# Performance work log

Measured on AMD Instinct MI355X. Metric: run time of the kernel, lower is better.

## Reference

```python
import jax, jax.numpy as jnp
import numpy as np

B, C, Q, E = 32, 1024, 64, 256  # batch, max_context_len, max_question_len, embedding_size
FE = 4 * E                      # final_encoding_size (self_attention=False)


def setup_inputs() -> dict:
    key = jax.random.key(0)
    ks = jax.random.split(key, 7)
    return {
        "context": jax.random.normal(ks[0], (B, C, E), dtype=jnp.float32),
        "question": jax.random.normal(ks[1], (B, Q, E), dtype=jnp.float32),
        "context_mask": jnp.ones((B, C), dtype=jnp.float32),
        "w_question": jax.random.normal(ks[2], (E,), dtype=jnp.float32),
        "w_context": jax.random.normal(ks[3], (E,), dtype=jnp.float32),
        "w_multiple": jax.random.normal(ks[4], (E,), dtype=jnp.float32),
        "final_W": jax.random.normal(ks[5], (FE, FE), dtype=jnp.float32) * (1.0 / np.sqrt(FE)),
        "final_b": jnp.zeros((FE,), dtype=jnp.float32),
    }


def reference(context, question, context_mask, w_question, w_context, w_multiple, final_W, final_b):
    # Trilinear similarity: s[b,c,q] = <w_q, q_q> + <w_c, c_c> + <w_m, c_c * q_q>
    q_weighted = question @ w_question                 # (B, Q)
    ctx_weighted = context @ w_context                 # (B, C)
    # (question.unsqueeze(1) * context.unsqueeze(2)) @ w_multiple, computed
    # without materializing the (B, C, Q, E) intermediate:
    mult = jnp.einsum('bce,bqe->bcq', context * w_multiple, question)  # (B, C, Q)
    similarity = ctx_weighted[:, :, None] + q_weighted[:, None, :] + mult  # (B, C, Q)

    # Context-to-query attention (softmax over question dim)
    c2q_att = jnp.einsum('bcq,bqe->bce', jax.nn.softmax(similarity, axis=2), question)

    # Query-to-context attention (softmax over context dim of row-max scores)
    q2c_weights = jax.nn.softmax(jnp.max(similarity, axis=2), axis=1)   # (B, C)
    q2c_att = jnp.einsum('bc,bce->be', q2c_weights, context)            # (B, E)

    attended = jnp.concatenate(
        [context, c2q_att, context * c2q_att, context * q2c_att[:, None, :]],
        axis=2)                                                          # (B, C, 4E)

    # MaskedLinear: affine map, output rows zeroed where context_mask == 0
    out = (attended @ final_W.T + final_b) * context_mask[:, :, None]    # (B, C, 4E)
    return out
```

## Files before the change

kernel.cpp:

```cpp
#include <hip/hip_runtime.h>

#define BB 32
#define CC 1024
#define QQ 64
#define EE 256
#define FE 1024
#define MM (BB*CC)

typedef __bf16 bf16_t;
typedef bf16_t bf16x8 __attribute__((ext_vector_type(8)));
typedef float f32x4 __attribute__((ext_vector_type(4)));
typedef unsigned short u16x8 __attribute__((ext_vector_type(8)));

__device__ __forceinline__ unsigned short f2bf(float f) {
  unsigned u = __float_as_uint(f);
  u += 0x7fffu + ((u >> 16) & 1u);
  return (unsigned short)(u >> 16);
}
__device__ __forceinline__ float bf2f(unsigned short u) {
  return __uint_as_float(((unsigned)u) << 16);
}

__device__ __forceinline__ void gload_lds16(const void* g, void* l) {
  __builtin_amdgcn_global_load_lds(
      (const __attribute__((address_space(1))) unsigned int*)g,
      (__attribute__((address_space(3))) unsigned int*)l, 16, 0, 0);
}

__global__ void k_prep(const float* __restrict__ question, const float* __restrict__ w_question,
                       float* __restrict__ qw,
                       const float* __restrict__ W, unsigned short* __restrict__ Wb) {
  int bx = blockIdx.x;
  if (bx < 512) {
    int gid = bx * 256 + threadIdx.x;
    int row = gid >> 6;
    int lane = gid & 63;
    const float4 q = *(const float4*)(question + (size_t)row * EE + lane * 4);
    const float4 wq = *(const float4*)(w_question + lane * 4);
    float d = q.x*wq.x + q.y*wq.y + q.z*wq.z + q.w*wq.w;
    d += __shfl_xor(d, 1);  d += __shfl_xor(d, 2);  d += __shfl_xor(d, 4);
    d += __shfl_xor(d, 8);  d += __shfl_xor(d, 16); d += __shfl_xor(d, 32);
    if (lane == 0) qw[row] = d;
  } else {
    int i = ((bx - 512) * 256 + threadIdx.x) * 4;
    float4 v = *(const float4*)(W + i);
    ushort4 o; o.x = f2bf(v.x); o.y = f2bf(v.y); o.z = f2bf(v.z); o.w = f2bf(v.w);
    *(ushort4*)(Wb + i) = o;
  }
}

#define DOT4(acc, A, Bv) acc += A.x*Bv.x + A.y*Bv.y + A.z*Bv.z + A.w*Bv.w

__launch_bounds__(256)
__global__ void k_simpv(const float* __restrict__ ctx, const float* __restrict__ question,
                        const float* __restrict__ qw_g, const float* __restrict__ w_context,
                        const float* __restrict__ w_multiple,
                        float* __restrict__ rowmax, unsigned short* __restrict__ att) {
  __shared__ float qbuf[QQ * 132];
  __shared__ float ck[64][36];
  __shared__ unsigned short Pl[QQ][68];
  __shared__ float cwl[64];
  __shared__ float qwl[QQ];
  const int tid = threadIdx.x;
  const int b = blockIdx.y;
  const int c0 = blockIdx.x * 64;
  const int tx = tid & 15, ty = tid >> 4;

  const float* qb = question + (size_t)b * (QQ * EE);
  if (tid < QQ) qwl[tid] = qw_g[b * QQ + tid];

  const int cr = tid >> 3, er = (tid & 7) * 4;
  const float* crow0 = ctx + ((size_t)(b * CC + c0 + cr)) * EE;
  const float* crow1 = crow0 + 32 * EE;
  unsigned short* arow0 = att + ((size_t)(b * CC + c0 + cr)) * FE;
  unsigned short* arow1 = arow0 + (size_t)32 * FE;
  float s[4][4] = {{0.f}};
  float cp0 = 0.f, cp1 = 0.f;

  for (int h = 0; h < 2; ++h) {
    if (h) __syncthreads();
    for (int idx = tid * 4; idx < QQ * 128; idx += 1024) {
      int row = idx >> 7, col = idx & 127;
      *(float4*)&qbuf[row * 132 + col] = *(const float4*)(qb + (size_t)row * EE + h * 128 + col);
    }
    for (int eo2 = 0; eo2 < 128; eo2 += 32) {
      const int eo = h * 128 + eo2;
      float4 cv0 = *(const float4*)(crow0 + eo + er);
      float4 cv1 = *(const float4*)(crow1 + eo + er);
      float4 wc = *(const float4*)(w_context + eo + er);
      float4 wm = *(const float4*)(w_multiple + eo + er);
      cp0 += cv0.x*wc.x + cv0.y*wc.y + cv0.z*wc.z + cv0.w*wc.w;
      cp1 += cv1.x*wc.x + cv1.y*wc.y + cv1.z*wc.z + cv1.w*wc.w;
      ushort4 u0, u1;
      u0.x = f2bf(cv0.x); u0.y = f2bf(cv0.y); u0.z = f2bf(cv0.z); u0.w = f2bf(cv0.w);
      u1.x = f2bf(cv1.x); u1.y = f2bf(cv1.y); u1.z = f2bf(cv1.z); u1.w = f2bf(cv1.w);
      *(ushort4*)(arow0 + eo + er) = u0;
      *(ushort4*)(arow1 + eo + er) = u1;
      __syncthreads();
      float4 m0, m1;
      m0.x = cv0.x*wm.x; m0.y = cv0.y*wm.y; m0.z = cv0.z*wm.z; m0.w = cv0.w*wm.w;
      m1.x = cv1.x*wm.x; m1.y = cv1.y*wm.y; m1.z = cv1.z*wm.z; m1.w = cv1.w*wm.w;
      *(float4*)&ck[cr][er] = m0;
      *(float4*)&ck[cr + 32][er] = m1;
      __syncthreads();
#pragma unroll
      for (int ee = 0; ee < 32; ee += 4) {
        float4 a0 = *(const float4*)&ck[ty +  0][ee];
        float4 a1 = *(const float4*)&ck[ty + 16][ee];
        float4 a2 = *(const float4*)&ck[ty + 32][ee];
        float4 a3 = *(const float4*)&ck[ty + 48][ee];
        float4 b0 = *(const float4*)&qbuf[(tx +  0) * 132 + eo2 + ee];
        float4 b1 = *(const float4*)&qbuf[(tx + 16) * 132 + eo2 + ee];
        float4 b2 = *(const float4*)&qbuf[(tx + 32) * 132 + eo2 + ee];
        float4 b3 = *(const float4*)&qbuf[(tx + 48) * 132 + eo2 + ee];
        DOT4(s[0][0], a0, b0); DOT4(s[0][1], a0, b1); DOT4(s[0][2], a0, b2); DOT4(s[0][3], a0, b3);
        DOT4(s[1][0], a1, b0); DOT4(s[1][1], a1, b1); DOT4(s[1][2], a1, b2); DOT4(s[1][3], a1, b3);
        DOT4(s[2][0], a2, b0); DOT4(s[2][1], a2, b1); DOT4(s[2][2], a2, b2); DOT4(s[2][3], a2, b3);
        DOT4(s[3][0], a3, b0); DOT4(s[3][1], a3, b1); DOT4(s[3][2], a3, b2); DOT4(s[3][3], a3, b3);
      }
    }
  }
  cp0 += __shfl_xor(cp0, 1); cp0 += __shfl_xor(cp0, 2); cp0 += __shfl_xor(cp0, 4);
  cp1 += __shfl_xor(cp1, 1); cp1 += __shfl_xor(cp1, 2); cp1 += __shfl_xor(cp1, 4);
  if ((tid & 7) == 0) { cwl[cr] = cp0; cwl[cr + 32] = cp1; }
  __syncthreads();

#pragma unroll
  for (int i = 0; i < 4; ++i) {
    int c = ty + 16 * i;
    float cw = cwl[c];
    float f[4], mx = -1e30f;
#pragma unroll
    for (int j = 0; j < 4; ++j) {
      f[j] = s[i][j] + cw + qwl[tx + 16 * j];
      mx = fmaxf(mx, f[j]);
    }
    mx = fmaxf(mx, __shfl_xor(mx, 1));
    mx = fmaxf(mx, __shfl_xor(mx, 2));
    mx = fmaxf(mx, __shfl_xor(mx, 4));
    mx = fmaxf(mx, __shfl_xor(mx, 8));
    float sum = 0.f;
#pragma unroll
    for (int j = 0; j < 4; ++j) { f[j] = expf(f[j] - mx); sum += f[j]; }
    sum += __shfl_xor(sum, 1);
    sum += __shfl_xor(sum, 2);
    sum += __shfl_xor(sum, 4);
    sum += __shfl_xor(sum, 8);
    float inv = 1.f / sum;
    if (tx == 0) rowmax[(size_t)b * CC + c0 + c] = mx;
#pragma unroll
    for (int j = 0; j < 4; ++j) Pl[tx + 16 * j][c] = f2bf(f[j] * inv);
  }
  __syncthreads();

  for (int ep = 0; ep < EE; ep += 64) {
    if (ep) __syncthreads();
    {
      int q = tid >> 2, e16 = (tid & 3) * 16;
      const float* src = qb + (size_t)q * EE + ep + e16;
      *(float4*)&qbuf[q * 68 + e16 +  0] = *(const float4*)(src);
      *(float4*)&qbuf[q * 68 + e16 +  4] = *(const float4*)(src + 4);
      *(float4*)&qbuf[q * 68 + e16 +  8] = *(const float4*)(src + 8);
      *(float4*)&qbuf[q * 68 + e16 + 12] = *(const float4*)(src + 12);
    }
    __syncthreads();
    float s2[4][4] = {{0.f}};
#pragma unroll 8
    for (int q = 0; q < QQ; ++q) {
      float a0 = bf2f(Pl[q][ty +  0]);
      float a1 = bf2f(Pl[q][ty + 16]);
      float a2 = bf2f(Pl[q][ty + 32]);
      float a3 = bf2f(Pl[q][ty + 48]);
      float4 bv = *(const float4*)&qbuf[q * 68 + tx * 4];
      s2[0][0] += a0 * bv.x; s2[0][1] += a0 * bv.y; s2[0][2] += a0 * bv.z; s2[0][3] += a0 * bv.w;
      s2[1][0] += a1 * bv.x; s2[1][1] += a1 * bv.y; s2[1][2] += a1 * bv.z; s2[1][3] += a1 * bv.w;
      s2[2][0] += a2 * bv.x; s2[2][1] += a2 * bv.y; s2[2][2] += a2 * bv.z; s2[2][3] += a2 * bv.w;
      s2[3][0] += a3 * bv.x; s2[3][1] += a3 * bv.y; s2[3][2] += a3 * bv.z; s2[3][3] += a3 * bv.w;
    }
#pragma unroll
    for (int i = 0; i < 4; ++i) {
      int c = ty + 16 * i;
      size_t row = (size_t)(b * CC + c0 + c);
      unsigned short* arow = att + row * (size_t)FE;
      ushort4 cu = *(const ushort4*)(arow + ep + tx * 4);
      float cx = bf2f(cu.x), cy = bf2f(cu.y), cz = bf2f(cu.z), cw = bf2f(cu.w);
      ushort4 o1, o2;
      o1.x = f2bf(s2[i][0]);       o1.y = f2bf(s2[i][1]);       o1.z = f2bf(s2[i][2]);       o1.w = f2bf(s2[i][3]);
      o2.x = f2bf(cx * s2[i][0]);  o2.y = f2bf(cy * s2[i][1]);  o2.z = f2bf(cz * s2[i][2]);  o2.w = f2bf(cw * s2[i][3]);
      *(ushort4*)(arow + 1 * EE + ep + tx * 4) = o1;
      *(ushort4*)(arow + 2 * EE + ep + tx * 4) = o2;
    }
  }
}

__global__ void k_q2c_softmax(const float* __restrict__ rowmax, float* __restrict__ q2cw) {
  int b = blockIdx.x, tid = threadIdx.x;
  __shared__ float rbuf[4], sbuf[4];
  float4 v = *(const float4*)(rowmax + (size_t)b * CC + tid * 4);
  float m = fmaxf(fmaxf(v.x, v.y), fmaxf(v.z, v.w));
  for (int off = 1; off < 64; off <<= 1) m = fmaxf(m, __shfl_xor(m, off));
  int wv = tid >> 6;
  if ((tid & 63) == 0) rbuf[wv] = m;
  __syncthreads();
  m = fmaxf(fmaxf(rbuf[0], rbuf[1]), fmaxf(rbuf[2], rbuf[3]));
  float e0 = expf(v.x - m), e1 = expf(v.y - m), e2 = expf(v.z - m), e3 = expf(v.w - m);
  float sum = e0 + e1 + e2 + e3;
  for (int off = 1; off < 64; off <<= 1) sum += __shfl_xor(sum, off);
  if ((tid & 63) == 0) sbuf[wv] = sum;
  __syncthreads();
  sum = sbuf[0] + sbuf[1] + sbuf[2] + sbuf[3];
  float inv = 1.f / sum;
  float4 o; o.x = e0 * inv; o.y = e1 * inv; o.z = e2 * inv; o.w = e3 * inv;
  *(float4*)(q2cw + (size_t)b * CC + tid * 4) = o;
}

__global__ void k_q2c_part(const unsigned short* __restrict__ att, const float* __restrict__ w,
                           float* __restrict__ part) {
  int b = blockIdx.y, ch = blockIdx.x;
  int e = threadIdx.x;
  const unsigned short* base = att + ((size_t)(b * CC + ch * 128)) * FE + e;
  const float* wp = w + b * CC + ch * 128;
  float acc = 0.f;
#pragma unroll 4
  for (int c = 0; c < 128; ++c) acc += wp[c] * bf2f(base[(size_t)c * FE]);
  part[(b * 8 + ch) * EE + e] = acc;
}

__global__ void k_q2c_sum(const float* __restrict__ part, float* __restrict__ q2catt) {
  int b = blockIdx.x, e = threadIdx.x;
  float a = 0.f;
#pragma unroll
  for (int ch = 0; ch < 8; ++ch) a += part[(b * 8 + ch) * EE + e];
  q2catt[b * EE + e] = a;
}

__global__ void k_att3(const unsigned short* __restrict__ att_ro, const float* __restrict__ q2catt,
                       unsigned short* __restrict__ att_wr) {
  int unit = blockIdx.x * 256 + threadIdx.x;
  int row = unit >> 5;
  int e8 = (unit & 31) * 8;
  int b = row >> 10;
  u16x8 c = *(const u16x8*)(att_ro + (size_t)row * FE + e8);
  float4 g0 = *(const float4*)(q2catt + b * EE + e8);
  float4 g1 = *(const float4*)(q2catt + b * EE + e8 + 4);
  u16x8 o;
  o[0] = f2bf(bf2f(c[0]) * g0.x); o[1] = f2bf(bf2f(c[1]) * g0.y);
  o[2] = f2bf(bf2f(c[2]) * g0.z); o[3] = f2bf(bf2f(c[3]) * g0.w);
  o[4] = f2bf(bf2f(c[4]) * g1.x); o[5] = f2bf(bf2f(c[5]) * g1.y);
  o[6] = f2bf(bf2f(c[6]) * g1.z); o[7] = f2bf(bf2f(c[7]) * g1.w);
  *(u16x8*)(att_wr + (size_t)row * FE + 3 * EE + e8) = o;
}

__launch_bounds__(512, 2)
__global__ void k_gemm(const unsigned short* __restrict__ A, const unsigned short* __restrict__ Bw,
                       const float* __restrict__ bias, const float* __restrict__ mask,
                       float* __restrict__ out) {
  __shared__ bf16_t As[2][2][128][64];
  __shared__ bf16_t Bs[2][2][128][64];
  const int tid = threadIdx.x;
  const int lane = tid & 63;
  const int wave = tid >> 6;
  const int wr = wave >> 2;
  const int wc = wave & 3;
  const int bh = wc >> 1;

  const int bid = blockIdx.x;
  const int wg = (bid & 7) * 64 + (bid >> 3);
  const int brow = (wg >> 2) * 256;
  const int bcol = (wg & 3) * 256;

  const int r = lane & 15, kg4 = lane >> 4;
  const int rx = r & 7;

  const int srow = tid >> 3;
  const int sg = (tid & 7) ^ (srow & 7);
  const unsigned short* gAb = A  + (size_t)(brow + srow) * FE + sg * 8;
  const unsigned short* gBb = Bw + (size_t)(bcol + srow) * FE + sg * 8;
  bf16_t* ldsAb = &As[0][0][srow][(tid & 7) * 8];
  bf16_t* ldsBb = &Bs[0][0][srow][(tid & 7) * 8];

  f32x4 acc[8][4] = {};
  bf16x8 faA[4][2], faB[4][2], fbA[2][2], fbB[2][2];

#define BARX __builtin_amdgcn_s_barrier()
#define VMW4 asm volatile("s_waitcnt vmcnt(4)" ::: "memory")
#define VMW0 asm volatile("s_waitcnt vmcnt(0)" ::: "memory")

#define ST_A(SLOT, H, KOFF) do {                                              \
    const unsigned short* s_ = gAb + (size_t)((H) * 128) * FE + (KOFF);       \
    bf16_t* d_ = ldsAb + ((SLOT) * 2 + (H)) * (128 * 64);                     \
    gload_lds16(s_, d_);                                                      \
    gload_lds16(s_ + (size_t)64 * FE, d_ + 64 * 64);                          \
  } while (0)
#define ST_B(SLOT, H, KOFF) do {                                              \
    const unsigned short* s_ = gBb + (size_t)((H) * 128) * FE + (KOFF);       \
    bf16_t* d_ = ldsBb + ((SLOT) * 2 + (H)) * (128 * 64);                     \
    gload_lds16(s_, d_);                                                      \
    gload_lds16(s_ + (size_t)64 * FE, d_ + 64 * 64);                          \
  } while (0)

#define RD_FA(DST, SLOT, MB) do {                                             \
    _Pragma("unroll") for (int mm = 0; mm < 4; ++mm) {                        \
      const int row_ = ((MB) + mm) * 16 + r;                                  \
      _Pragma("unroll") for (int ks = 0; ks < 2; ++ks)                        \
        DST[mm][ks] = *(const bf16x8*)&As[SLOT][wr][row_][((ks * 4 + kg4) ^ rx) * 8]; \
    } } while (0)
#define RD_FB(DST, SLOT, NB) do {                                             \
    _Pragma("unroll") for (int nn = 0; nn < 2; ++nn) {                        \
      const int row_ = (wc & 1) * 64 + ((NB) + nn) * 16 + r;                  \
      _Pragma("unroll") for (int ks = 0; ks < 2; ++ks)                        \
        DST[nn][ks] = *(const bf16x8*)&Bs[SLOT][bh][row_][((ks * 4 + kg4) ^ rx) * 8]; \
    } } while (0)

#define MFMA16(FA, FB, MB, NB) do {                                           \
    __builtin_amdgcn_s_setprio(1);                                            \
    _Pragma("unroll") for (int ks = 0; ks < 2; ++ks)                          \
    _Pragma("unroll") for (int mm = 0; mm < 4; ++mm)                          \
    _Pragma("unroll") for (int nn = 0; nn < 2; ++nn)                          \
      acc[(MB) + mm][(NB) + nn] = __builtin_amdgcn_mfma_f32_16x16x32_bf16(    \
          FA[mm][ks], FB[nn][ks], acc[(MB) + mm][(NB) + nn], 0, 0, 0);        \
    __builtin_amdgcn_s_setprio(0);                                            \
  } while (0)

  ST_B(0, 0, 0);  ST_B(0, 1, 0);  ST_A(0, 0, 0);  ST_A(0, 1, 0);
  ST_B(1, 0, 64); ST_B(1, 1, 64);
  VMW4;
  BARX;

#pragma unroll 1
  for (int i = 0; i < 8; ++i) {
    const int kT1 = (2 * i + 1) * 64;
    const int kT2 = (2 * i + 2) * 64;
    const int kT3 = (2 * i + 3) * 64;
    const bool more = (i < 7);

    RD_FA(faA, 0, 0); RD_FB(fbA, 0, 0);
    ST_A(1, 0, kT1);
    BARX; MFMA16(faA, fbA, 0, 0); BARX;
    RD_FB(fbB, 0, 2);
    ST_A(1, 1, kT1);
    BARX; MFMA16(faA, fbB, 0, 2); BARX;
    RD_FA(faB, 0, 4);
    if (more) ST_B(0, 0, kT2);
    BARX; MFMA16(faB, fbA, 4, 0); BARX;
    if (more) { ST_B(0, 1, kT2); VMW4; } else { VMW0; }
    BARX; MFMA16(faB, fbB, 4, 2); BARX;

    RD_FA(faA, 1, 0); RD_FB(fbA, 1, 0);
    if (more) ST_A(0, 0, kT2);
    BARX; MFMA16(faA, fbA, 0, 0); BARX;
    RD_FB(fbB, 1, 2);
    if (more) ST_A(0, 1, kT2);
    BARX; MFMA16(faA, fbB, 0, 2); BARX;
    RD_FA(faB, 1, 4);
    if (more) ST_B(1, 0, kT3);
    BARX; MFMA16(faB, fbA, 4, 0); BARX;
    if (more) { ST_B(1, 1, kT3); VMW4; }
    BARX; MFMA16(faB, fbB, 4, 2); BARX;
  }
#undef ST_A
#undef ST_B
#undef RD_FA
#undef RD_FB
#undef MFMA16

#pragma unroll
  for (int m = 0; m < 8; ++m) {
#pragma unroll
    for (int n = 0; n < 4; ++n) {
#pragma unroll
      for (int reg = 0; reg < 4; ++reg) {
        int row = brow + wr * 128 + m * 16 + kg4 * 4 + reg;
        int col = bcol + wc * 64 + n * 16 + r;
        out[(size_t)row * FE + col] = (acc[m][n][reg] + bias[col]) * mask[row];
      }
    }
  }
}

extern "C" void kernel_launch(void* const* d_in, const int* in_sizes, int n_in,
                              void* d_out, int out_size, void* d_ws, size_t ws_size,
                              hipStream_t stream) {
  const float* ctx  = (const float*)d_in[0];
  const float* ques = (const float*)d_in[1];
  const float* mask = (const float*)d_in[2];
  const float* w_q  = (const float*)d_in[3];
  const float* w_c  = (const float*)d_in[4];
  const float* w_m  = (const float*)d_in[5];
  const float* fW   = (const float*)d_in[6];
  const float* fb   = (const float*)d_in[7];
  float* out = (float*)d_out;

  char* ws = (char*)d_ws;
  float* qw     = (float*)(ws);
  float* rowmax = (float*)(ws + 8192);
  float* q2cw   = (float*)(ws + 139264);
  float* part   = (float*)(ws + 270336);
  float* q2catt = (float*)(ws + 532480);
  unsigned short* attended = (unsigned short*)(ws + 1048576);
  unsigned short* Wb       = (unsigned short*)(ws + 68157440);

  k_prep<<<1536, 256, 0, stream>>>(ques, w_q, qw, fW, Wb);
  k_simpv<<<dim3(16, 32), 256, 0, stream>>>(ctx, ques, qw, w_c, w_m, rowmax, attended);
  k_q2c_softmax<<<32, 256, 0, stream>>>(rowmax, q2cw);
  k_q2c_part<<<dim3(8, 32), 256, 0, stream>>>(attended, q2cw, part);
  k_q2c_sum<<<32, 256, 0, stream>>>(part, q2catt);
  k_att3<<<4096, 256, 0, stream>>>(attended, q2catt, attended);
  k_gemm<<<512, 512, 0, stream>>>(attended, Wb, fb, mask, out);
}
```

Baseline: 160.7 us.

## Replace pipelined 256x256 GEMM with simple single-buffered 128x128 tile kernel

Replaces the hand-scheduled, double-buffered 256x256-tile GEMM (512 threads, K-step 64, interleaved barriers and async LDS loads) with a plain 128x128-tile kernel using 256 threads, K-step 32, a single LDS buffer and two syncthreads per iteration. The grid grows from 512 to 2048 blocks, with more blocks allowed per CU. This trades away load/compute overlap and data reuse per tile for simpler code and more occupancy. It likely exposes global-load latency and doubles operand traffic.

```diff
diff --git a/kernel.cpp b/kernel.cpp
--- a/kernel.cpp
+++ b/kernel.cpp
@@ -251,126 +251,65 @@
   *(u16x8*)(att_wr + (size_t)row * FE + 3 * EE + e8) = o;
 }
 
-__launch_bounds__(512, 2)
+__launch_bounds__(256, 3)
 __global__ void k_gemm(const unsigned short* __restrict__ A, const unsigned short* __restrict__ Bw,
                        const float* __restrict__ bias, const float* __restrict__ mask,
                        float* __restrict__ out) {
-  __shared__ bf16_t As[2][2][128][64];
-  __shared__ bf16_t Bs[2][2][128][64];
+  __shared__ bf16_t As[128][32];
+  __shared__ bf16_t Bs[128][32];
   const int tid = threadIdx.x;
   const int lane = tid & 63;
   const int wave = tid >> 6;
-  const int wr = wave >> 2;
-  const int wc = wave & 3;
-  const int bh = wc >> 1;
+  const int wr = wave >> 1, wc = wave & 1;
 
   const int bid = blockIdx.x;
-  const int wg = (bid & 7) * 64 + (bid >> 3);
-  const int brow = (wg >> 2) * 256;
-  const int bcol = (wg & 3) * 256;
-
-  const int r = lane & 15, kg4 = lane >> 4;
-  const int rx = r & 7;
-
-  const int srow = tid >> 3;
-  const int sg = (tid & 7) ^ (srow & 7);
-  const unsigned short* gAb = A  + (size_t)(brow + srow) * FE + sg * 8;
-  const unsigned short* gBb = Bw + (size_t)(bcol + srow) * FE + sg * 8;
-  bf16_t* ldsAb = &As[0][0][srow][(tid & 7) * 8];
-  bf16_t* ldsBb = &Bs[0][0][srow][(tid & 7) * 8];
-
-  f32x4 acc[8][4] = {};
-  bf16x8 faA[4][2], faB[4][2], fbA[2][2], fbB[2][2];
-
-#define BARX __builtin_amdgcn_s_barrier()
-#define VMW4 asm volatile("s_waitcnt vmcnt(4)" ::: "memory")
-#define VMW0 asm volatile("s_waitcnt vmcnt(0)" ::: "memory")
-
-#define ST_A(SLOT, H, KOFF) do {                                              \
-    const unsigned short* s_ = gAb + (size_t)((H) * 128) * FE + (KOFF);       \
-    bf16_t* d_ = ldsAb + ((SLOT) * 2 + (H)) * (128 * 64);                     \
-    gload_lds16(s_, d_);                                                      \
-    gload_lds16(s_ + (size_t)64 * FE, d_ + 64 * 64);                          \
-  } while (0)
-#define ST_B(SLOT, H, KOFF) do {                                              \
-    const unsigned short* s_ = gBb + (size_t)((H) * 128) * FE + (KOFF);       \
-    bf16_t* d_ = ldsBb + ((SLOT) * 2 + (H)) * (128 * 64);                     \
-    gload_lds16(s_, d_);                                                      \
-    gload_lds16(s_ + (size_t)64 * FE, d_ + 64 * 64);                          \
-  } while (0)
-
-#define RD_FA(DST, SLOT, MB) do {                                             \
-    _Pragma("unroll") for (int mm = 0; mm < 4; ++mm) {                        \
-      const int row_ = ((MB) + mm) * 16 + r;                                  \
-      _Pragma("unroll") for (int ks = 0; ks < 2; ++ks)                        \
-        DST[mm][ks] = *(const bf16x8*)&As[SLOT][wr][row_][((ks * 4 + kg4) ^ rx) * 8]; \
-    } } while (0)
-#define RD_FB(DST, SLOT, NB) do {                                             \
-    _Pragma("unroll") for (int nn = 0; nn < 2; ++nn) {                        \
-      const int row_ = (wc & 1) * 64 + ((NB) + nn) * 16 + r;                  \
-      _Pragma("unroll") for (int ks = 0; ks < 2; ++ks)                        \
-        DST[nn][ks] = *(const bf16x8*)&Bs[SLOT][bh][row_][((ks * 4 + kg4) ^ rx) * 8]; \
-    } } while (0)
-
-#define MFMA16(FA, FB, MB, NB) do {                                           \
-    __builtin_amdgcn_s_setprio(1);                                            \
-    _Pragma("unroll") for (int ks = 0; ks < 2; ++ks)                          \
-    _Pragma("unroll") for (int mm = 0; mm < 4; ++mm)                          \
-    _Pragma("unroll") for (int nn = 0; nn < 2; ++nn)                          \
-      acc[(MB) + mm][(NB) + nn] = __builtin_amdgcn_mfma_f32_16x16x32_bf16(    \
-          FA[mm][ks], FB[nn][ks], acc[(MB) + mm][(NB) + nn], 0, 0, 0);        \
-    __builtin_amdgcn_s_setprio(0);                                            \
-  } while (0)
-
-  ST_B(0, 0, 0);  ST_B(0, 1, 0);  ST_A(0, 0, 0);  ST_A(0, 1, 0);
-  ST_B(1, 0, 64); ST_B(1, 1, 64);
-  VMW4;
-  BARX;
-
-#pragma unroll 1
-  for (int i = 0; i < 8; ++i) {
-    const int kT1 = (2 * i + 1) * 64;
-    const int kT2 = (2 * i + 2) * 64;
-    const int kT3 = (2 * i + 3) * 64;
-    const bool more = (i < 7);
-
-    RD_FA(faA, 0, 0); RD_FB(fbA, 0, 0);
-    ST_A(1, 0, kT1);
-    BARX; MFMA16(faA, fbA, 0, 0); BARX;
-    RD_FB(fbB, 0, 2);
-    ST_A(1, 1, kT1);
-    BARX; MFMA16(faA, fbB, 0, 2); BARX;
-    RD_FA(faB, 0, 4);
-    if (more) ST_B(0, 0, kT2);
-    BARX; MFMA16(faB, fbA, 4, 0); BARX;
-    if (more) { ST_B(0, 1, kT2); VMW4; } else { VMW0; }
-    BARX; MFMA16(faB, fbB, 4, 2); BARX;
-
-    RD_FA(faA, 1, 0); RD_FB(fbA, 1, 0);
-    if (more) ST_A(0, 0, kT2);
-    BARX; MFMA16(faA, fbA, 0, 0); BARX;
-    RD_FB(fbB, 1, 2);
-    if (more) ST_A(0, 1, kT2);
-    BARX; MFMA16(faA, fbB, 0, 2); BARX;
-    RD_FA(faB, 1, 4);
-    if (more) ST_B(1, 0, kT3);
-    BARX; MFMA16(faB, fbA, 4, 0); BARX;
-    if (more) { ST_B(1, 1, kT3); VMW4; }
-    BARX; MFMA16(faB, fbB, 4, 2); BARX;
-  }
-#undef ST_A
-#undef ST_B
-#undef RD_FA
-#undef RD_FB
-#undef MFMA16
-
-#pragma unroll
-  for (int m = 0; m < 8; ++m) {
+  const int wg = (bid & 7) * 256 + (bid >> 3);
+  const int bcol = (wg & 7) * 128;
+  const int brow = (wg >> 3) * 128;
+
+  const int r = lane & 15, kg = lane >> 4;
+  const int rk = (kg ^ (r & 3)) * 8;
+
+  const int srow = tid >> 2;
+  const int sgr = tid & 3;
+  const int ssw = (sgr ^ (srow & 3)) * 8;
+  const unsigned short* gA0 = A  + (size_t)(brow + srow) * FE + ssw;
+  const unsigned short* gA1 = gA0 + (size_t)64 * FE;
+  const unsigned short* gB0 = Bw + (size_t)(bcol + srow) * FE + ssw;
+  const unsigned short* gB1 = gB0 + (size_t)64 * FE;
+  bf16_t* dA0 = &As[srow][sgr * 8];
+  bf16_t* dA1 = dA0 + 64 * 32;
+  bf16_t* dB0 = &Bs[srow][sgr * 8];
+  bf16_t* dB1 = dB0 + 64 * 32;
+
+  f32x4 acc[4][4] = {};
+
+  for (int k0 = 0; k0 < FE; k0 += 32) {
+    gload_lds16(gA0 + k0, dA0);
+    gload_lds16(gA1 + k0, dA1);
+    gload_lds16(gB0 + k0, dB0);
+    gload_lds16(gB1 + k0, dB1);
+    __syncthreads();
+    bf16x8 fa[4], fb[4];
+#pragma unroll
+    for (int m = 0; m < 4; ++m) fa[m] = *(const bf16x8*)&As[wr * 64 + m * 16 + r][rk];
+#pragma unroll
+    for (int n = 0; n < 4; ++n) fb[n] = *(const bf16x8*)&Bs[wc * 64 + n * 16 + r][rk];
+#pragma unroll
+    for (int m = 0; m < 4; ++m)
+#pragma unroll
+      for (int n = 0; n < 4; ++n)
+        acc[m][n] = __builtin_amdgcn_mfma_f32_16x16x32_bf16(fa[m], fb[n], acc[m][n], 0, 0, 0);
+    __syncthreads();
+  }
+
+#pragma unroll
+  for (int m = 0; m < 4; ++m) {
 #pragma unroll
     for (int n = 0; n < 4; ++n) {
 #pragma unroll
       for (int reg = 0; reg < 4; ++reg) {
-        int row = brow + wr * 128 + m * 16 + kg4 * 4 + reg;
+        int row = brow + wr * 64 + m * 16 + kg * 4 + reg;
         int col = bcol + wc * 64 + n * 16 + r;
         out[(size_t)row * FE + col] = (acc[m][n][reg] + bias[col]) * mask[row];
       }
@@ -406,5 +345,5 @@
   k_q2c_part<<<dim3(8, 32), 256, 0, stream>>>(attended, q2cw, part);
   k_q2c_sum<<<32, 256, 0, stream>>>(part, q2catt);
   k_att3<<<4096, 256, 0, stream>>>(attended, q2catt, attended);
-  k_gemm<<<512, 512, 0, stream>>>(attended, Wb, fb, mask, out);
-}
+  k_gemm<<<2048, 256, 0, stream>>>(attended, Wb, fb, mask, out);
+}
```

After: 172.2 us. 1.07x slower.
